# Kernel tuning notes

Hardware: AMD Instinct MI355X
Metric: run time of the kernel (lower is better)

Reference implementation:

```python
import jax, jax.numpy as jnp
import numpy as np

# static multi-scale config (Deformable-DETR encoder, 1024x1024 image, strides 8/16/32/64)
SPATIAL_SHAPES = np.array([[128, 128], [64, 64], [32, 32], [16, 16]])  # (L, 2) = (h, w)
NUM_HEADS, NUM_LEVELS, NUM_POINTS = 8, 4, 4
EMBED, HEAD_DIM = 256, 32
NUM_KEYS = int(SPATIAL_SHAPES.prod(-1).sum())  # 21760


def _grid_sample(img, grid):
    """Bilinear grid_sample, padding_mode='zeros', align_corners=False.
    img: (BH, C, H, W); grid: (BH, Nq, P, 2) in [-1,1] -> (BH, C, Nq, P)."""
    BH, C, H, W = img.shape
    gx = (grid[..., 0] + 1.0) * (W / 2) - 0.5
    gy = (grid[..., 1] + 1.0) * (H / 2) - 0.5
    x0f, y0f = jnp.floor(gx), jnp.floor(gy)
    wx, wy = gx - x0f, gy - y0f
    x0, y0 = x0f.astype(jnp.int32), y0f.astype(jnp.int32)
    flat = img.reshape(BH, C, H * W)

    def gather(xi, yi, w):
        valid = (xi >= 0) & (xi < W) & (yi >= 0) & (yi < H)
        idx = jnp.clip(yi, 0, H - 1) * W + jnp.clip(xi, 0, W - 1)
        g = jnp.take_along_axis(flat, idx.reshape(BH, 1, -1), axis=2)
        g = g.reshape(BH, C, xi.shape[1], xi.shape[2])
        return g * (w * valid)[:, None]

    return (gather(x0, y0, (1 - wx) * (1 - wy)) + gather(x0 + 1, y0, wx * (1 - wy))
            + gather(x0, y0 + 1, (1 - wx) * wy) + gather(x0 + 1, y0 + 1, wx * wy))


def setup_inputs() -> dict:
    key = jax.random.key(0)
    ks = jax.random.split(key, 12)
    bs, nq = 1, NUM_KEYS
    s = 1.0 / np.sqrt(EMBED)
    return {
        "query": jax.random.normal(ks[0], (bs, nq, EMBED), jnp.float32),
        "query_pos": jax.random.normal(ks[1], (bs, nq, EMBED), jnp.float32),
        "value": jax.random.normal(ks[2], (bs, NUM_KEYS, EMBED), jnp.float32),
        "reference_points": jax.random.uniform(ks[3], (bs, nq, NUM_LEVELS, 2), jnp.float32),
        "spatial_shapes": jnp.asarray(SPATIAL_SHAPES, jnp.int32),
        "W_value": jax.random.normal(ks[4], (EMBED, EMBED), jnp.float32) * s,
        "b_value": jnp.zeros((EMBED,), jnp.float32),
        "W_off": jax.random.normal(ks[5], (NUM_HEADS * NUM_LEVELS * NUM_POINTS * 2, EMBED), jnp.float32) * 0.01,
        "b_off": jax.random.normal(ks[6], (NUM_HEADS * NUM_LEVELS * NUM_POINTS * 2,), jnp.float32),
        "W_attn": jax.random.normal(ks[7], (NUM_HEADS * NUM_LEVELS * NUM_POINTS, EMBED), jnp.float32) * s,
        "b_attn": jnp.zeros((NUM_HEADS * NUM_LEVELS * NUM_POINTS,), jnp.float32),
        "W_out": jax.random.normal(ks[8], (EMBED, EMBED), jnp.float32) * s,
        "b_out": jnp.zeros((EMBED,), jnp.float32),
    }


def reference(query, query_pos, value, reference_points, spatial_shapes,
              W_value, b_value, W_off, b_off, W_attn, b_attn, W_out, b_out):
    bs, nq, _ = query.shape
    identity = query
    q = query + query_pos  # pos_add
    v = value @ W_value.T + b_value  # value_proj: (bs, nk, E)
    v = v.reshape(bs, -1, NUM_HEADS, HEAD_DIM)

    offsets = (q @ W_off.T + b_off).reshape(bs, nq, NUM_HEADS, NUM_LEVELS, NUM_POINTS, 2)
    attn = (q @ W_attn.T + b_attn).reshape(bs, nq, NUM_HEADS, NUM_LEVELS * NUM_POINTS)
    attn = jax.nn.softmax(attn, axis=-1).reshape(bs, nq, NUM_HEADS, NUM_LEVELS, NUM_POINTS)

    # offset_normalizer = (w, h) per level; ref points are 2D -> loc = ref + off/norm
    normalizer = jnp.asarray(SPATIAL_SHAPES[:, ::-1].copy(), query.dtype)  # (L, 2)
    loc = reference_points[:, :, None, :, None, :] + offsets / normalizer[None, None, None, :, None, :]
    grids = 2.0 * loc - 1.0  # (bs, nq, H, L, P, 2)

    starts = np.concatenate([[0], np.cumsum(SPATIAL_SHAPES.prod(-1))])
    sampled = []
    for lvl in range(NUM_LEVELS):
        H_, W_ = int(SPATIAL_SHAPES[lvl, 0]), int(SPATIAL_SHAPES[lvl, 1])
        v_l = v[:, int(starts[lvl]):int(starts[lvl + 1])]  # (bs, H*W, heads, Dh)
        v_l = v_l.transpose(0, 2, 3, 1).reshape(bs * NUM_HEADS, HEAD_DIM, H_, W_)
        g_l = grids[:, :, :, lvl].transpose(0, 2, 1, 3, 4).reshape(bs * NUM_HEADS, nq, NUM_POINTS, 2)
        sampled.append(_grid_sample(v_l, g_l))  # (bs*H, Dh, nq, P)
    sampled = jnp.concatenate(sampled, axis=-1)  # (bs*H, Dh, nq, L*P)

    aw = attn.transpose(0, 2, 1, 3, 4).reshape(bs * NUM_HEADS, 1, nq, NUM_LEVELS * NUM_POINTS)
    out = (sampled * aw).sum(-1).reshape(bs, NUM_HEADS * HEAD_DIM, nq).transpose(0, 2, 1)
    out = out @ W_out.T + b_out  # output_proj
    return out + identity  # residual (dropout is identity at eval)
```

## Files before the change

kernel.cpp:

```cpp
#include <hip/hip_runtime.h>
#include <hip/hip_bf16.h>
#include <math.h>
#include <type_traits>

#define K_DIM 256
using bf16 = __hip_bfloat16;

typedef __attribute__((ext_vector_type(8))) short s8v;
typedef __attribute__((ext_vector_type(4))) float f4v;

__device__ __forceinline__ float b2f(unsigned short u) {
    return __uint_as_float(((unsigned)u) << 16);
}
__device__ __forceinline__ unsigned short f2b(float f) {
    unsigned u = __float_as_uint(f);
    unsigned r = 0x7FFFu + ((u >> 16) & 1u);
    return (unsigned short)((u + r) >> 16);
}
__device__ __forceinline__ float  ld1(const float* p) { return *p; }
__device__ __forceinline__ float  ld1(const bf16*  p) { return b2f(*(const unsigned short*)p); }
__device__ __forceinline__ void   st1(float* p, float v) { *p = v; }
__device__ __forceinline__ void   st1(bf16*  p, float v) { *(unsigned short*)p = f2b(v); }
__device__ __forceinline__ float4 ld4(const float* p) { return *(const float4*)p; }
__device__ __forceinline__ float4 ld4(const bf16*  p) {
    ushort4 u = *(const ushort4*)p;
    return make_float4(b2f(u.x), b2f(u.y), b2f(u.z), b2f(u.w));
}
__device__ __forceinline__ s8v ldw8(const bf16* p) { return *(const s8v*)p; }

__device__ __forceinline__ bool detect_bf16(const unsigned* __restrict__ qw) {
    unsigned w = qw[threadIdx.x & 63];
    unsigned t = (w >> 8) & 0x7F;
    bool hit = (t >= 0x3Bu) && (t <= 0x42u);
    unsigned long long m = __ballot(hit);
    return __popcll(m) >= 32;
}

#define P1_TOTAL 164480
__global__ __launch_bounds__(256) void k_prep1(
    const unsigned* __restrict__ qd,
    const void* wv, const void* wo, const void* wa,
    const void* bv, const void* bo, const void* ba, bf16* __restrict__ dst)
{
    const bool isb = detect_bf16(qd);
    const int i4 = (blockIdx.x * 256 + threadIdx.x) * 4;
    if (i4 >= P1_TOTAL) return;
    const void* src; int off;
    if      (i4 < 65536)  { src = wv; off = i4; }
    else if (i4 < 131072) { src = wo; off = i4 - 65536; }
    else if (i4 < 163840) { src = wa; off = i4 - 131072; }
    else if (i4 < 164096) { src = bv; off = i4 - 163840; }
    else if (i4 < 164352) { src = bo; off = i4 - 164096; }
    else                  { src = ba; off = i4 - 164352; }
    if (isb) {
        *(ushort4*)(dst + i4) = *(const ushort4*)((const unsigned short*)src + off);
    } else {
        float4 v = *(const float4*)((const float*)src + off);
        *(ushort4*)(dst + i4) = make_ushort4(f2b(v.x), f2b(v.y), f2b(v.z), f2b(v.w));
    }
}

#define P2_TOTAL 65792
__global__ __launch_bounds__(256) void k_prep2(
    const unsigned* __restrict__ qd,
    const void* wout, const void* bout, bf16* __restrict__ dst)
{
    const bool isb = detect_bf16(qd);
    const int i4 = (blockIdx.x * 256 + threadIdx.x) * 4;
    if (i4 >= P2_TOTAL) return;
    const void* src; int off;
    if (i4 < 65536) { src = wout; off = i4; }
    else            { src = bout; off = i4 - 65536; }
    if (isb) {
        *(ushort4*)(dst + i4) = *(const ushort4*)((const unsigned short*)src + off);
    } else {
        float4 v = *(const float4*)((const float*)src + off);
        *(ushort4*)(dst + i4) = make_ushort4(f2b(v.x), f2b(v.y), f2b(v.z), f2b(v.w));
    }
}

template<typename AT, typename RT, typename CT, int NFRAG, bool ADD_A2, bool SPLIT, bool ADD_RES>
__device__ __forceinline__ void mfma_gemm_body(
    unsigned short* __restrict__ As,
    const AT* __restrict__ A1, const AT* __restrict__ A2,
    const bf16* __restrict__ W1, const bf16* __restrict__ bias1, CT* __restrict__ C1, int N1,
    const bf16* __restrict__ W2, const bf16* __restrict__ bias2, bf16* __restrict__ C2, int N2,
    const RT* __restrict__ Res)
{
    const int tid = threadIdx.x;
    const int bm = blockIdx.x * 32;

    {
        const AT* t1 = A1 + (size_t)bm * K_DIM;
        if constexpr (!ADD_A2 && std::is_same<AT, bf16>::value) {
            #pragma unroll
            for (int j = 0; j < 4; ++j) {
                const int e = j * 2048 + tid * 8;
                const int row = e >> 8, col = e & 255;
                *(s8v*)&As[row * 264 + col] = *(const s8v*)(t1 + e);
            }
        } else {
            const AT* t2 = ADD_A2 ? (A2 + (size_t)bm * K_DIM) : (const AT*)0;
            #pragma unroll
            for (int j = 0; j < 8; ++j) {
                const int e = j * 1024 + tid * 4;
                float4 v = ld4(t1 + e);
                if (ADD_A2) {
                    float4 w2 = ld4(t2 + e);
                    v.x += w2.x; v.y += w2.y; v.z += w2.z; v.w += w2.w;
                }
                const int row = e >> 8, col = e & 255;
                *(ushort4*)&As[row * 264 + col] =
                    make_ushort4(f2b(v.x), f2b(v.y), f2b(v.z), f2b(v.w));
            }
        }
    }
    __syncthreads();

    const int wv = tid >> 6;
    const int lane = tid & 63;
    const int n15 = lane & 15;
    const int quad = lane >> 4;

    const bf16* Wr[NFRAG];
    int col[NFRAG];
    #pragma unroll
    for (int f = 0; f < NFRAG; ++f) {
        const int c = (wv * NFRAG + f) * 16 + n15;
        col[f] = c;
        if (SPLIT && c >= N1) Wr[f] = W2 + (size_t)(c - N1) * K_DIM;
        else                  Wr[f] = W1 + (size_t)c * K_DIM;
    }

    const f4v zz = {0.f, 0.f, 0.f, 0.f};
    f4v acc[2][NFRAG];
    #pragma unroll
    for (int mi = 0; mi < 2; ++mi)
        #pragma unroll
        for (int f = 0; f < NFRAG; ++f) acc[mi][f] = zz;

    #pragma unroll
    for (int kk = 0; kk < 8; ++kk) {
        const int k0 = kk * 32 + quad * 8;
        s8v b[NFRAG];
        #pragma unroll
        for (int f = 0; f < NFRAG; ++f) b[f] = ldw8(Wr[f] + k0);
        s8v a[2];
        #pragma unroll
        for (int mi = 0; mi < 2; ++mi)
            a[mi] = *(const s8v*)&As[(mi * 16 + n15) * 264 + k0];
        #pragma unroll
        for (int mi = 0; mi < 2; ++mi)
            #pragma unroll
            for (int f = 0; f < NFRAG; ++f)
                acc[mi][f] = __builtin_amdgcn_mfma_f32_16x16x32_bf16(a[mi], b[f], acc[mi][f], 0, 0, 0);
    }

    #pragma unroll
    for (int f = 0; f < NFRAG; ++f) {
        const int c = col[f];
        const bool hi = SPLIT && (c >= N1);
        const float bv = hi ? ld1(bias2 + (c - N1)) : ld1(bias1 + c);
        #pragma unroll
        for (int mi = 0; mi < 2; ++mi)
            #pragma unroll
            for (int r = 0; r < 4; ++r) {
                const int m = bm + mi * 16 + quad * 4 + r;
                float v = acc[mi][f][r] + bv;
                if (ADD_RES) v += ld1(Res + (size_t)m * N1 + c);
                if (hi) st1(C2 + (size_t)m * N2 + (c - N1), v);
                else    st1(C1 + (size_t)m * N1 + c, v);
            }
    }
}

template<int NFRAG, bool ADD_A2, bool SPLIT>
__global__ __launch_bounds__(256) void k_gemm(
    const unsigned* __restrict__ qd, const void* A1, const void* A2,
    const bf16* W1, const bf16* b1, bf16* C1, int N1,
    const bf16* W2, const bf16* b2, bf16* C2, int N2)
{
    __shared__ unsigned short As[32 * 264];
    if (detect_bf16(qd))
        mfma_gemm_body<bf16, float, bf16, NFRAG, ADD_A2, SPLIT, false>(As,
            (const bf16*)A1, (const bf16*)A2, W1, b1, C1, N1, W2, b2, C2, N2, nullptr);
    else
        mfma_gemm_body<float, float, bf16, NFRAG, ADD_A2, SPLIT, false>(As,
            (const float*)A1, (const float*)A2, W1, b1, C1, N1, W2, b2, C2, N2, nullptr);
}

__global__ __launch_bounds__(256) void k_gemm_final(
    const unsigned* __restrict__ qd, const bf16* A1,
    const bf16* W, const bf16* bias, const void* Res, void* C)
{
    __shared__ unsigned short As[32 * 264];
    if (detect_bf16(qd))
        mfma_gemm_body<bf16, bf16, bf16, 4, false, false, true>(As,
            A1, nullptr, W, bias, (bf16*)C, 256,
            nullptr, nullptr, nullptr, 0, (const bf16*)Res);
    else
        mfma_gemm_body<bf16, float, float, 4, false, false, true>(As,
            A1, nullptr, W, bias, (float*)C, 256,
            nullptr, nullptr, nullptr, 0, (const float*)Res);
}

struct SampLds {
    float    sofs[4][256];
    float    slog[4][128];
    float    sref[4][8];
    float    swgt[4][128][4];
    unsigned sidx[4][128][4];
};

__global__ __launch_bounds__(256) void k_sample(
    const unsigned* __restrict__ qd, const bf16* __restrict__ vproj,
    bf16* __restrict__ osb, const bf16* __restrict__ logits,
    const void* __restrict__ refp)
{
    __shared__ SampLds L;
    const bool isb = detect_bf16(qd);
    const int t = threadIdx.x;
    const int qg = t >> 6;
    const int t64 = t & 63;
    const int q = blockIdx.x * 4 + qg;

    {
        ushort4 u = *(const ushort4*)(osb + (size_t)q * 256 + t64 * 4);
        *(float4*)&L.sofs[qg][t64 * 4] = make_float4(b2f(u.x), b2f(u.y), b2f(u.z), b2f(u.w));
    }
    L.slog[qg][t64]      = ld1(logits + (size_t)q * 128 + t64);
    L.slog[qg][t64 + 64] = ld1(logits + (size_t)q * 128 + t64 + 64);
    if (t64 < 8)
        L.sref[qg][t64] = isb ? ld1((const bf16*)refp + (size_t)q * 8 + t64)
                              : ld1((const float*)refp + (size_t)q * 8 + t64);
    __syncthreads();

    if (t64 < 8) {
        float m = -1e30f;
        #pragma unroll
        for (int i = 0; i < 16; ++i) m = fmaxf(m, L.slog[qg][t64 * 16 + i]);
        float e[16];
        float s = 0.f;
        #pragma unroll
        for (int i = 0; i < 16; ++i) { e[i] = __expf(L.slog[qg][t64 * 16 + i] - m); s += e[i]; }
        const float inv = 1.f / s;
        #pragma unroll
        for (int i = 0; i < 16; ++i) L.slog[qg][t64 * 16 + i] = e[i] * inv;
    }
    __syncthreads();

    {
        const int hh = t64 & 7;
        const int i2 = t64 >> 3;
        #pragma unroll
        for (int tt = 0; tt < 2; ++tt) {
            const int i = i2 * 2 + tt;
            const int l = i >> 2;
            const int p = i & 3;
            const int WW = 128 >> l;
            const int st = (l == 0) ? 0 : (l == 1) ? 16384 : (l == 2) ? 20480 : 21504;
            const float ox = L.sofs[qg][hh * 32 + l * 8 + p * 2 + 0];
            const float oy = L.sofs[qg][hh * 32 + l * 8 + p * 2 + 1];
            const float gx = L.sref[qg][l * 2 + 0] * (float)WW + ox - 0.5f;
            const float gy = L.sref[qg][l * 2 + 1] * (float)WW + oy - 0.5f;
            const float x0f = floorf(gx);
            const float y0f = floorf(gy);
            const float wx = gx - x0f;
            const float wy = gy - y0f;
            const int x0 = (int)x0f;
            const int y0 = (int)y0f;
            const float aw = L.slog[qg][hh * 16 + i];
            const float vx0 = (x0 >= 0 && x0 < WW) ? 1.f : 0.f;
            const float vx1 = (x0 + 1 >= 0 && x0 + 1 < WW) ? 1.f : 0.f;
            const float vy0 = (y0 >= 0 && y0 < WW) ? 1.f : 0.f;
            const float vy1 = (y0 + 1 >= 0 && y0 + 1 < WW) ? 1.f : 0.f;
            const int xc0 = min(max(x0, 0), WW - 1);
            const int xc1 = min(max(x0 + 1, 0), WW - 1);
            const int yc0 = min(max(y0, 0), WW - 1);
            const int yc1 = min(max(y0 + 1, 0), WW - 1);
            const int slot = t64 + (tt << 6);
            *(float4*)L.swgt[qg][slot] = make_float4(
                (1.f - wx) * (1.f - wy) * aw * vx0 * vy0,
                wx * (1.f - wy) * aw * vx1 * vy0,
                (1.f - wx) * wy * aw * vx0 * vy1,
                wx * wy * aw * vx1 * vy1);
            *(uint4*)L.sidx[qg][slot] = make_uint4(
                (unsigned)(st + yc0 * WW + xc0) * 512u,
                (unsigned)(st + yc0 * WW + xc1) * 512u,
                (unsigned)(st + yc1 * WW + xc0) * 512u,
                (unsigned)(st + yc1 * WW + xc1) * 512u);
        }
    }
    __syncthreads();

    const int h = t64 >> 3;
    const int dg = t64 & 7;
    const unsigned chb = (unsigned)(h * 32 + dg * 4) * 2u;
    const char* vb = (const char*)vproj;
    float a0 = 0.f, a1 = 0.f, a2 = 0.f, a3 = 0.f;
    #pragma unroll
    for (int i = 0; i < 16; ++i) {
        const int slot = ((i >> 1) << 3) | h | ((i & 1) << 6);
        const uint4  iv = *(const uint4*)L.sidx[qg][slot];
        const float4 wv = *(const float4*)L.swgt[qg][slot];
        {
            ushort4 pv = *(const ushort4*)(vb + (size_t)(iv.x + chb));
            a0 = fmaf(wv.x, b2f(pv.x), a0); a1 = fmaf(wv.x, b2f(pv.y), a1);
            a2 = fmaf(wv.x, b2f(pv.z), a2); a3 = fmaf(wv.x, b2f(pv.w), a3);
        }
        {
            ushort4 pv = *(const ushort4*)(vb + (size_t)(iv.y + chb));
            a0 = fmaf(wv.y, b2f(pv.x), a0); a1 = fmaf(wv.y, b2f(pv.y), a1);
            a2 = fmaf(wv.y, b2f(pv.z), a2); a3 = fmaf(wv.y, b2f(pv.w), a3);
        }
        {
            ushort4 pv = *(const ushort4*)(vb + (size_t)(iv.z + chb));
            a0 = fmaf(wv.z, b2f(pv.x), a0); a1 = fmaf(wv.z, b2f(pv.y), a1);
            a2 = fmaf(wv.z, b2f(pv.z), a2); a3 = fmaf(wv.z, b2f(pv.w), a3);
        }
        {
            ushort4 pv = *(const ushort4*)(vb + (size_t)(iv.w + chb));
            a0 = fmaf(wv.w, b2f(pv.x), a0); a1 = fmaf(wv.w, b2f(pv.y), a1);
            a2 = fmaf(wv.w, b2f(pv.z), a2); a3 = fmaf(wv.w, b2f(pv.w), a3);
        }
    }
    *(ushort4*)(osb + (size_t)q * 256 + h * 32 + dg * 4) =
        make_ushort4(f2b(a0), f2b(a1), f2b(a2), f2b(a3));
}

extern "C" void kernel_launch(void* const* d_in, const int* in_sizes, int n_in,
                              void* d_out, int out_size, void* d_ws, size_t ws_size,
                              hipStream_t stream) {
    const void* query     = d_in[0];
    const void* query_pos = d_in[1];
    const void* value     = d_in[2];
    const void* refp      = d_in[3];
    const void* W_value = d_in[5];
    const void* b_value = d_in[6];
    const void* W_off   = d_in[7];
    const void* b_off   = d_in[8];
    const void* W_attn  = d_in[9];
    const void* b_attn  = d_in[10];
    const void* W_out   = d_in[11];
    const void* b_out   = d_in[12];
    const unsigned* qd = (const unsigned*)d_in[0];

    const int M = in_sizes[0] / 256;
    char* wsb = (char*)d_ws;

    bf16* vproj = (bf16*)wsb;
    bf16* osb   = (bf16*)(wsb + (size_t)M * 512);
    bf16* logit = (bf16*)d_out;
    bf16* wc1   = (bf16*)((char*)d_out + (8u << 20));
    const bf16* c_wv = wc1;
    const bf16* c_wo = wc1 + 65536;
    const bf16* c_wa = wc1 + 131072;
    const bf16* c_bv = wc1 + 163840;
    const bf16* c_bo = wc1 + 164096;
    const bf16* c_ba = wc1 + 164352;
    bf16* wc2 = vproj;

    dim3 blk(256, 1, 1);
    dim3 g32((unsigned)(M / 32), 1, 1);
    dim3 gs((unsigned)(M / 4), 1, 1);

    k_prep1<<<dim3((P1_TOTAL / 4 + 255) / 256), blk, 0, stream>>>(qd,
        W_value, W_off, W_attn, b_value, b_off, b_attn, wc1);
    k_gemm<4, false, false><<<g32, blk, 0, stream>>>(qd, value, nullptr,
        c_wv, c_bv, vproj, 256, nullptr, nullptr, nullptr, 0);
    k_gemm<6, true, true><<<g32, blk, 0, stream>>>(qd, query, query_pos,
        c_wo, c_bo, osb, 256, c_wa, c_ba, logit, 128);
    k_sample<<<gs, blk, 0, stream>>>(qd, vproj, osb, logit, refp);
    k_prep2<<<dim3((P2_TOTAL / 4 + 255) / 256), blk, 0, stream>>>(qd, W_out, b_out, wc2);
    k_gemm_final<<<g32, blk, 0, stream>>>(qd, osb, wc2, wc2 + 65536, query, d_out);
}
```

Baseline: 237.9 us.

## Store projected values head-major and compute softmax/offsets in registers via shuffles

```diff
diff --git a/kernel.cpp b/kernel.cpp
--- a/kernel.cpp
+++ b/kernel.cpp
@@ -79,13 +79,13 @@
     }
 }
 
-template<typename AT, typename RT, typename CT, int NFRAG, bool ADD_A2, bool SPLIT, bool ADD_RES>
+template<typename AT, typename RT, typename CT, int NFRAG, bool ADD_A2, bool SPLIT, bool ADD_RES, bool HMAJOR>
 __device__ __forceinline__ void mfma_gemm_body(
     unsigned short* __restrict__ As,
     const AT* __restrict__ A1, const AT* __restrict__ A2,
     const bf16* __restrict__ W1, const bf16* __restrict__ bias1, CT* __restrict__ C1, int N1,
     const bf16* __restrict__ W2, const bf16* __restrict__ bias2, bf16* __restrict__ C2, int N2,
-    const RT* __restrict__ Res)
+    const RT* __restrict__ Res, int Mtot)
 {
     const int tid = threadIdx.x;
     const int bm = blockIdx.x * 32;
@@ -161,6 +161,8 @@
         const int c = col[f];
         const bool hi = SPLIT && (c >= N1);
         const float bv = hi ? ld1(bias2 + (c - N1)) : ld1(bias1 + c);
+        size_t hbase = 0;
+        if (HMAJOR) hbase = (size_t)(c >> 5) * (size_t)Mtot * 32 + (c & 31);
         #pragma unroll
         for (int mi = 0; mi < 2; ++mi)
             #pragma unroll
@@ -168,25 +170,26 @@
                 const int m = bm + mi * 16 + quad * 4 + r;
                 float v = acc[mi][f][r] + bv;
                 if (ADD_RES) v += ld1(Res + (size_t)m * N1 + c);
-                if (hi) st1(C2 + (size_t)m * N2 + (c - N1), v);
-                else    st1(C1 + (size_t)m * N1 + c, v);
+                if (hi)          st1(C2 + (size_t)m * N2 + (c - N1), v);
+                else if (HMAJOR) st1(C1 + hbase + (size_t)m * 32, v);
+                else             st1(C1 + (size_t)m * N1 + c, v);
             }
     }
 }
 
-template<int NFRAG, bool ADD_A2, bool SPLIT>
+template<int NFRAG, bool ADD_A2, bool SPLIT, bool HMAJOR>
 __global__ __launch_bounds__(256) void k_gemm(
     const unsigned* __restrict__ qd, const void* A1, const void* A2,
     const bf16* W1, const bf16* b1, bf16* C1, int N1,
-    const bf16* W2, const bf16* b2, bf16* C2, int N2)
+    const bf16* W2, const bf16* b2, bf16* C2, int N2, int Mtot)
 {
     __shared__ unsigned short As[32 * 264];
     if (detect_bf16(qd))
-        mfma_gemm_body<bf16, float, bf16, NFRAG, ADD_A2, SPLIT, false>(As,
-            (const bf16*)A1, (const bf16*)A2, W1, b1, C1, N1, W2, b2, C2, N2, nullptr);
+        mfma_gemm_body<bf16, float, bf16, NFRAG, ADD_A2, SPLIT, false, HMAJOR>(As,
+            (const bf16*)A1, (const bf16*)A2, W1, b1, C1, N1, W2, b2, C2, N2, nullptr, Mtot);
     else
-        mfma_gemm_body<float, float, bf16, NFRAG, ADD_A2, SPLIT, false>(As,
-            (const float*)A1, (const float*)A2, W1, b1, C1, N1, W2, b2, C2, N2, nullptr);
+        mfma_gemm_body<float, float, bf16, NFRAG, ADD_A2, SPLIT, false, HMAJOR>(As,
+            (const float*)A1, (const float*)A2, W1, b1, C1, N1, W2, b2, C2, N2, nullptr, Mtot);
 }
 
 __global__ __launch_bounds__(256) void k_gemm_final(
@@ -195,19 +198,16 @@
 {
     __shared__ unsigned short As[32 * 264];
     if (detect_bf16(qd))
-        mfma_gemm_body<bf16, bf16, bf16, 4, false, false, true>(As,
+        mfma_gemm_body<bf16, bf16, bf16, 4, false, false, true, false>(As,
             A1, nullptr, W, bias, (bf16*)C, 256,
-            nullptr, nullptr, nullptr, 0, (const bf16*)Res);
+            nullptr, nullptr, nullptr, 0, (const bf16*)Res, 0);
     else
-        mfma_gemm_body<bf16, float, float, 4, false, false, true>(As,
+        mfma_gemm_body<bf16, float, float, 4, false, false, true, false>(As,
             A1, nullptr, W, bias, (float*)C, 256,
-            nullptr, nullptr, nullptr, 0, (const float*)Res);
+            nullptr, nullptr, nullptr, 0, (const float*)Res, 0);
 }
 
 struct SampLds {
-    float    sofs[4][256];
-    float    slog[4][128];
-    float    sref[4][8];
     float    swgt[4][128][4];
     unsigned sidx[4][128][4];
 };
@@ -215,7 +215,7 @@
 __global__ __launch_bounds__(256) void k_sample(
     const unsigned* __restrict__ qd, const bf16* __restrict__ vproj,
     bf16* __restrict__ osb, const bf16* __restrict__ logits,
-    const void* __restrict__ refp)
+    const void* __restrict__ refp, int Mtot)
 {
     __shared__ SampLds L;
     const bool isb = detect_bf16(qd);
@@ -224,78 +224,91 @@
     const int t64 = t & 63;
     const int q = blockIdx.x * 4 + qg;
 
+    float f0, f1, f2, f3;
     {
         ushort4 u = *(const ushort4*)(osb + (size_t)q * 256 + t64 * 4);
-        *(float4*)&L.sofs[qg][t64 * 4] = make_float4(b2f(u.x), b2f(u.y), b2f(u.z), b2f(u.w));
-    }
-    L.slog[qg][t64]      = ld1(logits + (size_t)q * 128 + t64);
-    L.slog[qg][t64 + 64] = ld1(logits + (size_t)q * 128 + t64 + 64);
-    if (t64 < 8)
-        L.sref[qg][t64] = isb ? ld1((const bf16*)refp + (size_t)q * 8 + t64)
-                              : ld1((const float*)refp + (size_t)q * 8 + t64);
+        f0 = b2f(u.x); f1 = b2f(u.y); f2 = b2f(u.z); f3 = b2f(u.w);
+    }
+
+    float p0, p1;
+    {
+        ushort2 lu = *(const ushort2*)(logits + (size_t)q * 128 + t64 * 2);
+        float l0 = b2f(lu.x), l1 = b2f(lu.y);
+        float mx = fmaxf(l0, l1);
+        mx = fmaxf(mx, __shfl_xor(mx, 1));
+        mx = fmaxf(mx, __shfl_xor(mx, 2));
+        mx = fmaxf(mx, __shfl_xor(mx, 4));
+        float e0 = __expf(l0 - mx), e1 = __expf(l1 - mx);
+        float s = e0 + e1;
+        s += __shfl_xor(s, 1);
+        s += __shfl_xor(s, 2);
+        s += __shfl_xor(s, 4);
+        const float inv = 1.f / s;
+        p0 = e0 * inv; p1 = e1 * inv;
+    }
+
+    const int hh  = t64 & 7;
+    const int i2  = t64 >> 3;
+    const int src = (hh << 3) | i2;
+    const float o0 = __shfl(f0, src);
+    const float o1 = __shfl(f1, src);
+    const float o2 = __shfl(f2, src);
+    const float o3 = __shfl(f3, src);
+    const float pa = __shfl(p0, src);
+    const float pb = __shfl(p1, src);
+
+    const int lv = i2 >> 1;
+    float rx, ry;
+    if (isb) {
+        rx = ld1((const bf16*)refp + (size_t)q * 8 + 2 * lv);
+        ry = ld1((const bf16*)refp + (size_t)q * 8 + 2 * lv + 1);
+    } else {
+        rx = ld1((const float*)refp + (size_t)q * 8 + 2 * lv);
+        ry = ld1((const float*)refp + (size_t)q * 8 + 2 * lv + 1);
+    }
+
+    #pragma unroll
+    for (int tt = 0; tt < 2; ++tt) {
+        const int i = i2 * 2 + tt;
+        const int l = i >> 2;
+        const int WW = 128 >> l;
+        const int st = (l == 0) ? 0 : (l == 1) ? 16384 : (l == 2) ? 20480 : 21504;
+        const float ox = tt ? o2 : o0;
+        const float oy = tt ? o3 : o1;
+        const float aw = tt ? pb : pa;
+        const float gx = rx * (float)WW + ox - 0.5f;
+        const float gy = ry * (float)WW + oy - 0.5f;
+        const float x0f = floorf(gx);
+        const float y0f = floorf(gy);
+        const float wx = gx - x0f;
+        const float wy = gy - y0f;
+        const int x0 = (int)x0f;
+        const int y0 = (int)y0f;
+        const float vx0 = (x0 >= 0 && x0 < WW) ? 1.f : 0.f;
+        const float vx1 = (x0 + 1 >= 0 && x0 + 1 < WW) ? 1.f : 0.f;
+        const float vy0 = (y0 >= 0 && y0 < WW) ? 1.f : 0.f;
+        const float vy1 = (y0 + 1 >= 0 && y0 + 1 < WW) ? 1.f : 0.f;
+        const int xc0 = min(max(x0, 0), WW - 1);
+        const int xc1 = min(max(x0 + 1, 0), WW - 1);
+        const int yc0 = min(max(y0, 0), WW - 1);
+        const int yc1 = min(max(y0 + 1, 0), WW - 1);
+        const int slot = t64 + (tt << 6);
+        *(float4*)L.swgt[qg][slot] = make_float4(
+            (1.f - wx) * (1.f - wy) * aw * vx0 * vy0,
+            wx * (1.f - wy) * aw * vx1 * vy0,
+            (1.f - wx) * wy * aw * vx0 * vy1,
+            wx * wy * aw * vx1 * vy1);
+        *(uint4*)L.sidx[qg][slot] = make_uint4(
+            (unsigned)(st + yc0 * WW + xc0) * 64u,
+            (unsigned)(st + yc0 * WW + xc1) * 64u,
+            (unsigned)(st + yc1 * WW + xc0) * 64u,
+            (unsigned)(st + yc1 * WW + xc1) * 64u);
+    }
     __syncthreads();
 
-    if (t64 < 8) {
-        float m = -1e30f;
-        #pragma unroll
-        for (int i = 0; i < 16; ++i) m = fmaxf(m, L.slog[qg][t64 * 16 + i]);
-        float e[16];
-        float s = 0.f;
-        #pragma unroll
-        for (int i = 0; i < 16; ++i) { e[i] = __expf(L.slog[qg][t64 * 16 + i] - m); s += e[i]; }
-        const float inv = 1.f / s;
-        #pragma unroll
-        for (int i = 0; i < 16; ++i) L.slog[qg][t64 * 16 + i] = e[i] * inv;
-    }
-    __syncthreads();
-
-    {
-        const int hh = t64 & 7;
-        const int i2 = t64 >> 3;
-        #pragma unroll
-        for (int tt = 0; tt < 2; ++tt) {
-            const int i = i2 * 2 + tt;
-            const int l = i >> 2;
-            const int p = i & 3;
-            const int WW = 128 >> l;
-            const int st = (l == 0) ? 0 : (l == 1) ? 16384 : (l == 2) ? 20480 : 21504;
-            const float ox = L.sofs[qg][hh * 32 + l * 8 + p * 2 + 0];
-            const float oy = L.sofs[qg][hh * 32 + l * 8 + p * 2 + 1];
-            const float gx = L.sref[qg][l * 2 + 0] * (float)WW + ox - 0.5f;
-            const float gy = L.sref[qg][l * 2 + 1] * (float)WW + oy - 0.5f;
-            const float x0f = floorf(gx);
-            const float y0f = floorf(gy);
-            const float wx = gx - x0f;
-            const float wy = gy - y0f;
-            const int x0 = (int)x0f;
-            const int y0 = (int)y0f;
-            const float aw = L.slog[qg][hh * 16 + i];
-            const float vx0 = (x0 >= 0 && x0 < WW) ? 1.f : 0.f;
-            const float vx1 = (x0 + 1 >= 0 && x0 + 1 < WW) ? 1.f : 0.f;
-            const float vy0 = (y0 >= 0 && y0 < WW) ? 1.f : 0.f;
-            const float vy1 = (y0 + 1 >= 0 && y0 + 1 < WW) ? 1.f : 0.f;
-            const int xc0 = min(max(x0, 0), WW - 1);
-            const int xc1 = min(max(x0 + 1, 0), WW - 1);
-            const int yc0 = min(max(y0, 0), WW - 1);
-            const int yc1 = min(max(y0 + 1, 0), WW - 1);
-            const int slot = t64 + (tt << 6);
-            *(float4*)L.swgt[qg][slot] = make_float4(
-                (1.f - wx) * (1.f - wy) * aw * vx0 * vy0,
-                wx * (1.f - wy) * aw * vx1 * vy0,
-                (1.f - wx) * wy * aw * vx0 * vy1,
-                wx * wy * aw * vx1 * vy1);
-            *(uint4*)L.sidx[qg][slot] = make_uint4(
-                (unsigned)(st + yc0 * WW + xc0) * 512u,
-                (unsigned)(st + yc0 * WW + xc1) * 512u,
-                (unsigned)(st + yc1 * WW + xc0) * 512u,
-                (unsigned)(st + yc1 * WW + xc1) * 512u);
-        }
-    }
-    __syncthreads();
-
-    const int h = t64 >> 3;
+    const int h  = t64 >> 3;
     const int dg = t64 & 7;
-    const unsigned chb = (unsigned)(h * 32 + dg * 4) * 2u;
+    const unsigned hb = (unsigned)(h * Mtot) * 64u + (unsigned)dg * 8u;
     const char* vb = (const char*)vproj;
     float a0 = 0.f, a1 = 0.f, a2 = 0.f, a3 = 0.f;
     #pragma unroll
@@ -304,22 +317,22 @@
         const uint4  iv = *(const uint4*)L.sidx[qg][slot];
         const float4 wv = *(const float4*)L.swgt[qg][slot];
         {
-            ushort4 pv = *(const ushort4*)(vb + (size_t)(iv.x + chb));
+            ushort4 pv = *(const ushort4*)(vb + (size_t)(iv.x + hb));
             a0 = fmaf(wv.x, b2f(pv.x), a0); a1 = fmaf(wv.x, b2f(pv.y), a1);
             a2 = fmaf(wv.x, b2f(pv.z), a2); a3 = fmaf(wv.x, b2f(pv.w), a3);
         }
         {
-            ushort4 pv = *(const ushort4*)(vb + (size_t)(iv.y + chb));
+            ushort4 pv = *(const ushort4*)(vb + (size_t)(iv.y + hb));
             a0 = fmaf(wv.y, b2f(pv.x), a0); a1 = fmaf(wv.y, b2f(pv.y), a1);
             a2 = fmaf(wv.y, b2f(pv.z), a2); a3 = fmaf(wv.y, b2f(pv.w), a3);
         }
         {
-            ushort4 pv = *(const ushort4*)(vb + (size_t)(iv.z + chb));
+            ushort4 pv = *(const ushort4*)(vb + (size_t)(iv.z + hb));
             a0 = fmaf(wv.z, b2f(pv.x), a0); a1 = fmaf(wv.z, b2f(pv.y), a1);
             a2 = fmaf(wv.z, b2f(pv.z), a2); a3 = fmaf(wv.z, b2f(pv.w), a3);
         }
         {
-            ushort4 pv = *(const ushort4*)(vb + (size_t)(iv.w + chb));
+            ushort4 pv = *(const ushort4*)(vb + (size_t)(iv.w + hb));
             a0 = fmaf(wv.w, b2f(pv.x), a0); a1 = fmaf(wv.w, b2f(pv.y), a1);
             a2 = fmaf(wv.w, b2f(pv.z), a2); a3 = fmaf(wv.w, b2f(pv.w), a3);
         }
@@ -366,11 +379,11 @@
 
     k_prep1<<<dim3((P1_TOTAL / 4 + 255) / 256), blk, 0, stream>>>(qd,
         W_value, W_off, W_attn, b_value, b_off, b_attn, wc1);
-    k_gemm<4, false, false><<<g32, blk, 0, stream>>>(qd, value, nullptr,
-        c_wv, c_bv, vproj, 256, nullptr, nullptr, nullptr, 0);
-    k_gemm<6, true, true><<<g32, blk, 0, stream>>>(qd, query, query_pos,
-        c_wo, c_bo, osb, 256, c_wa, c_ba, logit, 128);
-    k_sample<<<gs, blk, 0, stream>>>(qd, vproj, osb, logit, refp);
+    k_gemm<4, false, false, true><<<g32, blk, 0, stream>>>(qd, value, nullptr,
+        c_wv, c_bv, vproj, 256, nullptr, nullptr, nullptr, 0, M);
+    k_gemm<6, true, true, false><<<g32, blk, 0, stream>>>(qd, query, query_pos,
+        c_wo, c_bo, osb, 256, c_wa, c_ba, logit, 128, M);
+    k_sample<<<gs, blk, 0, stream>>>(qd, vproj, osb, logit, refp, M);
     k_prep2<<<dim3((P2_TOTAL / 4 + 255) / 256), blk, 0, stream>>>(qd, W_out, b_out, wc2);
     k_gemm_final<<<g32, blk, 0, stream>>>(qd, osb, wc2, wc2 + 65536, query, d_out);
 }
```

New measurement: 232.2 us. 1.02x faster.
